# Kernel optimization log

Hardware: AMD Instinct MI355X
Metric: run time of the kernel (lower is better)

The kernel has to match this reference:

```python
import jax, jax.numpy as jnp
import numpy as np

D = 128; H = 4; C = 128; L = 4
NC = 65536   # cells (1024 graphs x 64 cells)
NP = 32768   # pieces
NE = 65536   # edges per cell->cell direction
B = 1024     # num graphs
BW = 7       # BOARD_WIDTH (undefined global in source; connect-four width)
SLOPE = 0.2  # GATv2 LeakyReLU negative slope


def setup_inputs() -> dict:
    key = jax.random.key(0)
    ks = jax.random.split(key, 24)
    s = 0.05
    return {
        'cell_x': jnp.zeros((NC,), dtype=jnp.int32),
        'piece_x': jax.random.randint(ks[0], (NP,), 0, 2, dtype=jnp.int32),
        'occ_src': jax.random.randint(ks[1], (NP,), 0, NP, dtype=jnp.int32),
        'occ_dst': jax.random.randint(ks[2], (NP,), 0, NC, dtype=jnp.int32),
        'en_src': jax.random.randint(ks[3], (NE,), 0, NC, dtype=jnp.int32),
        'en_dst': jax.random.randint(ks[4], (NE,), 0, NC, dtype=jnp.int32),
        'ee_src': jax.random.randint(ks[5], (NE,), 0, NC, dtype=jnp.int32),
        'ee_dst': jax.random.randint(ks[6], (NE,), 0, NC, dtype=jnp.int32),
        'cell_batch': (jnp.arange(NC, dtype=jnp.int32) // (NC // B)).astype(jnp.int32),
        'cell_emb': jax.random.normal(ks[7], (1, D), jnp.float32),
        'piece_emb': jax.random.normal(ks[8], (2, D), jnp.float32),
        'Wl': jax.random.normal(ks[9], (L, 3, D, H * C), jnp.float32) * s,
        'bl': jnp.zeros((L, 3, H * C), jnp.float32),
        'Wr': jax.random.normal(ks[10], (L, 3, D, H * C), jnp.float32) * s,
        'br': jnp.zeros((L, 3, H * C), jnp.float32),
        'att': jax.random.normal(ks[11], (L, 3, H, C), jnp.float32) * 0.1,
        'conv_bias': jnp.zeros((L, 3, C), jnp.float32),
        'fc1_W': jax.random.normal(ks[12], (D, 64), jnp.float32) * s,
        'fc1_b': jnp.zeros((64,), jnp.float32),
        'pol_W': jax.random.normal(ks[13], (64, BW), jnp.float32) * s,
        'pol_b': jnp.zeros((BW,), jnp.float32),
        'val_W': jax.random.normal(ks[14], (64, 1), jnp.float32) * s,
        'val_b': jnp.zeros((1,), jnp.float32),
    }


def _gatv2(x_src, x_dst, src, dst, Wl, bl, Wr, br, att, bias):
    # PyG GATv2Conv, concat=False (mean over heads), add_self_loops=False, eval-mode dropout.
    n_dst = x_dst.shape[0]
    xl = (x_src @ Wl + bl).reshape(-1, H, C)      # [Ns,H,C]
    xr = (x_dst @ Wr + br).reshape(n_dst, H, C)   # [Nd,H,C]
    e = jax.nn.leaky_relu(xl[src] + xr[dst], SLOPE)            # [E,H,C]
    score = jnp.einsum('ehc,hc->eh', e, att)                   # [E,H]
    m = jax.ops.segment_max(score, dst, num_segments=n_dst)    # [Nd,H]
    p = jnp.exp(score - m[dst])
    denom = jax.ops.segment_sum(p, dst, num_segments=n_dst)
    alpha = p / (denom[dst] + 1e-16)                           # scatter-softmax
    out = jax.ops.segment_sum(alpha[:, :, None] * xl[src], dst, num_segments=n_dst)  # [Nd,H,C]
    return out.mean(axis=1) + bias


def reference(cell_x, piece_x, occ_src, occ_dst, en_src, en_dst, ee_src, ee_dst,
              cell_batch, cell_emb, piece_emb, Wl, bl, Wr, br, att, conv_bias,
              fc1_W, fc1_b, pol_W, pol_b, val_W, val_b):
    cell = cell_emb[cell_x]    # [NC,D]
    piece = piece_emb[piece_x]  # [NP,D]
    rels = [(occ_src, occ_dst), (en_src, en_dst), (ee_src, ee_dst)]
    for l in range(L):
        acc = jnp.zeros_like(cell)
        for r, (src, dst) in enumerate(rels):
            x_src = piece if r == 0 else cell
            acc = acc + _gatv2(x_src, cell, src, dst, Wl[l, r], bl[l, r],
                               Wr[l, r], br[l, r], att[l, r], conv_bias[l, r])
        cell = jax.nn.relu(acc)  # HeteroConv aggr='sum', then relu; dropout is identity in eval
    # global mean pool over cells per graph
    sums = jax.ops.segment_sum(cell, cell_batch, num_segments=B)
    cnts = jax.ops.segment_sum(jnp.ones((cell.shape[0],), cell.dtype), cell_batch, num_segments=B)
    pooled = sums / jnp.maximum(cnts, 1.0)[:, None]            # [B,D]
    h = jax.nn.relu(pooled @ fc1_W + fc1_b)
    policy_logits = h @ pol_W + pol_b
    value = jnp.tanh(h @ val_W + val_b)
    return policy_logits, value
```

## Files before the change

kernel.cpp:

```cpp
#include <hip/hip_runtime.h>
#include <hip/hip_bf16.h>
#include <math.h>

#define NCELLS 65536
#define NPIECE 32768
#define NEDGE  65536
#define NGRAPH 1024
#define DIM    128
#define NH     4
#define CH     128
#define HC     512
#define NLAYER 4
#define SLOPE  0.2f
#define DCAP   16

#define SCAP0   16384
#define SCAP12  36864
#define HCAP0   8192
#define HCAP12  20480
#define XLC_OFF0 0
#define XLC_OFF1 16384
#define XLC_OFF2 53248
#define XRC_OFF0 0
#define XRC_OFF1 8192
#define XRC_OFF2 28672
#define YL_OFF0  0
#define YL_OFF1  32768
#define YL_OFF2  98304
#define GEMM_BLOCKS 5632

typedef __attribute__((ext_vector_type(8))) __bf16 bf16x8;
typedef __attribute__((ext_vector_type(4))) float f32x4;

__device__ inline float bf2f(unsigned int u) {
    return __uint_as_float(u << 16);
}
__device__ inline unsigned short f2bf(float f) {
    unsigned int x = __float_as_uint(f);
    unsigned int r = (x + 0x7fff + ((x >> 16) & 1)) >> 16;
    return (unsigned short)r;
}

#define GLOBAL_AS __attribute__((address_space(1)))
#define LDS_AS __attribute__((address_space(3)))
__device__ __forceinline__ void async_cp16(const void* g, void* l) {
    __builtin_amdgcn_global_load_lds((const GLOBAL_AS unsigned int*)g,
                                     (LDS_AS unsigned int*)l, 16, 0, 0);
}

__global__ void fill_kernel(float* __restrict__ p, float v, long n) {
    long i = (long)blockIdx.x * 256 + threadIdx.x;
    if (i < n) p[i] = v;
}

__global__ void embed_bf16_kernel(const int* __restrict__ idx, const float* __restrict__ emb,
                                  unsigned short* __restrict__ outb) {
    long t = (long)blockIdx.x * 256 + threadIdx.x;
    int node = (int)(t >> 7);
    int c = (int)(t & 127);
    outb[t] = f2bf(emb[(size_t)idx[node] * DIM + c]);
}

__global__ __launch_bounds__(256) void wconv_kernel(const float* __restrict__ Wl,
                                                    const float* __restrict__ Wr,
                                                    unsigned short* __restrict__ Wt) {
    __shared__ float tile[16][17];
    int bid = blockIdx.x;
    int wi = bid >> 8;
    int rem = bid & 255;
    int kt = rem >> 5;
    int nt = rem & 31;
    int tx = threadIdx.x & 15, ty = threadIdx.x >> 4;
    const float* W = (wi < 12) ? (Wl + (size_t)wi * DIM * HC) : (Wr + (size_t)(wi - 12) * DIM * HC);
    tile[ty][tx] = W[(size_t)(kt * 16 + ty) * HC + nt * 16 + tx];
    __syncthreads();
    Wt[(size_t)wi * HC * DIM + (size_t)(nt * 16 + ty) * DIM + kt * 16 + tx] = f2bf(tile[tx][ty]);
}

__global__ __launch_bounds__(256) void wsum_kernel(const float* __restrict__ Wl,
                                                   const float* __restrict__ bl,
                                                   unsigned short* __restrict__ Wsumt,
                                                   float* __restrict__ bsum) {
    int wi = blockIdx.x;
    const float* W = Wl + (size_t)wi * DIM * HC;
    for (int base = 0; base < 16384; base += 256) {
        int idx = base + threadIdx.x;
        int c = idx & 127, k = idx >> 7;
        float s = 0.25f * (W[(size_t)k * HC + c] + W[(size_t)k * HC + 128 + c] +
                           W[(size_t)k * HC + 256 + c] + W[(size_t)k * HC + 384 + c]);
        Wsumt[(size_t)wi * 16384 + (size_t)c * 128 + k] = f2bf(s);
    }
    if (threadIdx.x < 128) {
        int c = threadIdx.x;
        const float* b = bl + (size_t)wi * HC;
        bsum[wi * 128 + c] = 0.25f * (b[c] + b[128 + c] + b[256 + c] + b[384 + c]);
    }
}

__global__ __launch_bounds__(256) void bucket_build(const int* __restrict__ occ_src,
                                                    const int* __restrict__ occ_dst,
                                                    const int* __restrict__ en_src,
                                                    const int* __restrict__ en_dst,
                                                    const int* __restrict__ ee_src,
                                                    const int* __restrict__ ee_dst,
                                                    int* __restrict__ cnt3,
                                                    int* __restrict__ bucket3) {
    int id = blockIdx.x * 256 + threadIdx.x;
    int rel, e;
    const int* dstp;
    const int* srcp;
    if (id < NPIECE) { rel = 0; e = id; dstp = occ_dst; srcp = occ_src; }
    else if (id < NPIECE + NEDGE) { rel = 1; e = id - NPIECE; dstp = en_dst; srcp = en_src; }
    else if (id < NPIECE + 2 * NEDGE) { rel = 2; e = id - NPIECE - NEDGE; dstp = ee_dst; srcp = ee_src; }
    else return;
    int d = dstp[e];
    int pos = atomicAdd(&cnt3[rel * NCELLS + d], 1);
    if (pos < DCAP) bucket3[(size_t)rel * NCELLS * DCAP + (size_t)d * DCAP + pos] = srcp[e];
}

__global__ __launch_bounds__(256) void srcmark_build(const int* __restrict__ occ_src,
                                                     const int* __restrict__ occ_dst,
                                                     const int* __restrict__ en_src,
                                                     const int* __restrict__ en_dst,
                                                     const int* __restrict__ ee_src,
                                                     const int* __restrict__ ee_dst,
                                                     const int* __restrict__ cnt3,
                                                     int* __restrict__ srcmark) {
    int id = blockIdx.x * 256 + threadIdx.x;
    int rel, e;
    const int* dstp;
    const int* srcp;
    if (id < NPIECE) { rel = 0; e = id; dstp = occ_dst; srcp = occ_src; }
    else if (id < NPIECE + NEDGE) { rel = 1; e = id - NPIECE; dstp = en_dst; srcp = en_src; }
    else if (id < NPIECE + 2 * NEDGE) { rel = 2; e = id - NPIECE - NEDGE; dstp = ee_dst; srcp = ee_src; }
    else return;
    if (cnt3[rel * NCELLS + dstp[e]] >= 2) srcmark[(rel << 16) + srcp[e]] = 1;
}

__global__ __launch_bounds__(256) void hot_build(const int* __restrict__ cnt3,
                                                 int* __restrict__ counts,
                                                 int* __restrict__ hotlist,
                                                 int* __restrict__ hotpos) {
    int id = blockIdx.x * 256 + threadIdx.x;
    if (id >= 3 * NCELLS) return;
    int lane = threadIdx.x & 63;
    int r = id >> 16;
    int cap  = (r == 0) ? HCAP0 : HCAP12;
    int loff = (r == 0) ? XRC_OFF0 : (r == 1) ? XRC_OFF1 : XRC_OFF2;
    bool active = (cnt3[id] >= 2);
    unsigned long long mask = __ballot(active);
    if (mask) {
        int base = 0;
        if (lane == 0) base = atomicAdd(&counts[r], __popcll(mask));
        base = __shfl(base, 0, 64);
        if (active) {
            int pos = base + (int)__popcll(mask & ((1ull << lane) - 1ull));
            if (pos < cap) {
                hotlist[loff + pos] = id & (NCELLS - 1);
                hotpos[id] = pos;
            } else {
                hotpos[id] = cap - 1;
            }
        }
    }
}

__global__ __launch_bounds__(256) void src_compact(const int* __restrict__ srcmark,
                                                   int* __restrict__ counts,
                                                   int* __restrict__ srclist,
                                                   int* __restrict__ srcpos) {
    int id = blockIdx.x * 256 + threadIdx.x;
    if (id >= 3 * NCELLS) return;
    int lane = threadIdx.x & 63;
    int r = id >> 16;
    int cap  = (r == 0) ? SCAP0 : SCAP12;
    int loff = (r == 0) ? XLC_OFF0 : (r == 1) ? XLC_OFF1 : XLC_OFF2;
    bool active = (srcmark[id] != 0);
    unsigned long long mask = __ballot(active);
    if (mask) {
        int base = 0;
        if (lane == 0) base = atomicAdd(&counts[4 + r], __popcll(mask));
        base = __shfl(base, 0, 64);
        if (active) {
            int pos = base + (int)__popcll(mask & ((1ull << lane) - 1ull));
            if (pos < cap) {
                srclist[loff + pos] = id & (NCELLS - 1);
                srcpos[id] = pos;
            } else {
                srcpos[id] = cap - 1;
            }
        }
    }
}

__device__ __forceinline__ void gemm_body(const unsigned short* __restrict__ A,
                                          const int* __restrict__ gather, int nrows,
                                          const unsigned short* __restrict__ Bt,
                                          const float* __restrict__ bias,
                                          unsigned short* __restrict__ out, int ostride,
                                          int row0, int col0,
                                          unsigned short* smem) {
    unsigned short* As = smem;
    unsigned short* Bs = smem + 16384;
    const int t = threadIdx.x;
    const int w = t >> 6;
    const int l = t & 63;
    const int q = l >> 4, r15 = l & 15;

    {
#pragma unroll
        for (int it = 0; it < 8; it++) {
            int r0 = 32 * w + 4 * it;
            int row = r0 + q;
            int c = r15 ^ (row & 15);
            int grow = row0 + row;
            if (gather) grow = gather[grow < nrows ? grow : (nrows - 1)];
            async_cp16(A + (size_t)grow * 128 + c * 8, &As[r0 * 128]);
        }
        const unsigned short* Bg = Bt + (size_t)col0 * 128;
#pragma unroll
        for (int it = 0; it < 4; it++) {
            int r0 = 16 * w + 4 * it;
            int row = r0 + q;
            int c = r15 ^ (row & 15);
            async_cp16(Bg + (size_t)row * 128 + c * 8, &Bs[r0 * 128]);
        }
    }
    __syncthreads();

    const int m0 = (w >> 1) * 64;
    const int n0 = (w & 1) * 32;

    f32x4 acc[2][4][2];
#pragma unroll
    for (int nh = 0; nh < 2; nh++)
#pragma unroll
        for (int i = 0; i < 4; i++)
#pragma unroll
            for (int j = 0; j < 2; j++) acc[nh][i][j] = (f32x4)(0.0f);

#pragma unroll
    for (int ks = 0; ks < 4; ks++) {
        int slot = (4 * ks + q) ^ r15;
        bf16x8 a[4], b[2];
#pragma unroll
        for (int i = 0; i < 4; i++)
            a[i] = *(const bf16x8*)&As[(m0 + 16 * i + r15) * 128 + slot * 8];
#pragma unroll
        for (int j = 0; j < 2; j++)
            b[j] = *(const bf16x8*)&Bs[(n0 + 16 * j + r15) * 128 + slot * 8];
#pragma unroll
        for (int i = 0; i < 4; i++)
#pragma unroll
            for (int j = 0; j < 2; j++)
                acc[0][i][j] = __builtin_amdgcn_mfma_f32_16x16x32_bf16(a[i], b[j], acc[0][i][j], 0, 0, 0);
    }
    __syncthreads();

    {
        const unsigned short* Bg = Bt + (size_t)(col0 + 64) * 128;
#pragma unroll
        for (int it = 0; it < 4; it++) {
            int r0 = 16 * w + 4 * it;
            int row = r0 + q;
            int c = r15 ^ (row & 15);
            async_cp16(Bg + (size_t)row * 128 + c * 8, &Bs[r0 * 128]);
        }
    }
    __syncthreads();

#pragma unroll
    for (int ks = 0; ks < 4; ks++) {
        int slot = (4 * ks + q) ^ r15;
        bf16x8 a[4], b[2];
#pragma unroll
        for (int i = 0; i < 4; i++)
            a[i] = *(const bf16x8*)&As[(m0 + 16 * i + r15) * 128 + slot * 8];
#pragma unroll
        for (int j = 0; j < 2; j++)
            b[j] = *(const bf16x8*)&Bs[(n0 + 16 * j + r15) * 128 + slot * 8];
#pragma unroll
        for (int i = 0; i < 4; i++)
#pragma unroll
            for (int j = 0; j < 2; j++)
                acc[1][i][j] = __builtin_amdgcn_mfma_f32_16x16x32_bf16(a[i], b[j], acc[1][i][j], 0, 0, 0);
    }
    __syncthreads();

    unsigned short* tile = smem;
#pragma unroll
    for (int nh = 0; nh < 2; nh++)
#pragma unroll
        for (int j = 0; j < 2; j++) {
            int col = nh * 64 + n0 + 16 * j + r15;
            float bv = bias[col0 + col];
#pragma unroll
            for (int i = 0; i < 4; i++) {
                int mg = m0 + 16 * i + 4 * q;
#pragma unroll
                for (int rg = 0; rg < 4; rg++)
                    tile[(mg + rg) * 136 + col] = f2bf(acc[nh][i][j][rg] + bv);
            }
        }
    __syncthreads();
#pragma unroll
    for (int it = 0; it < 8; it++) {
        int rr = it * 16 + (t >> 4);
        int cc = (t & 15) * 8;
        if (row0 + rr < nrows) {
            uint4 v = *(const uint4*)&tile[rr * 136 + cc];
            *(uint4*)&out[(size_t)(row0 + rr) * ostride + col0 + cc] = v;
        }
    }
}

__global__ __launch_bounds__(256) void gemm_layer(const unsigned short* __restrict__ pieceb,
                                                  const unsigned short* __restrict__ cellb,
                                                  const int* __restrict__ srclist,
                                                  const int* __restrict__ hotlist,
                                                  const int* __restrict__ counts,
                                                  const unsigned short* __restrict__ Wt,
                                                  const unsigned short* __restrict__ Wsumt,
                                                  const float* __restrict__ bl,
                                                  const float* __restrict__ br,
                                                  const float* __restrict__ bsum,
                                                  unsigned short* __restrict__ xlc,
                                                  unsigned short* __restrict__ yl,
                                                  unsigned short* __restrict__ xrc,
                                                  int lay) {
    __shared__ unsigned short smem[24576];
    int x = blockIdx.x;
    int r, sec, idx;
    if (x < 1024) {
        r = 0;
        if (x < 512) { sec = 0; idx = x; }
        else if (x < 768) { sec = 1; idx = x - 512; }
        else { sec = 2; idx = x - 768; }
    } else if (x < 3328) {
        r = 1; x -= 1024;
        if (x < 1152) { sec = 0; idx = x; }
        else if (x < 1664) { sec = 1; idx = x - 1152; }
        else { sec = 2; idx = x - 1664; }
    } else {
        r = 2; x -= 3328;
        if (x < 1152) { sec = 0; idx = x; }
        else if (x < 1664) { sec = 1; idx = x - 1152; }
        else { sec = 2; idx = x - 1664; }
    }
    int wi = lay * 3 + r;
    const unsigned short* Asrc = (r == 0) ? pieceb : cellb;
    int Ns = (r == 0) ? NPIECE : NCELLS;
    int scap = (r == 0) ? SCAP0 : SCAP12;
    int hcap = (r == 0) ? HCAP0 : HCAP12;
    int xlcoff = (r == 0) ? XLC_OFF0 : (r == 1) ? XLC_OFF1 : XLC_OFF2;
    int xrcoff = (r == 0) ? XRC_OFF0 : (r == 1) ? XRC_OFF1 : XRC_OFF2;
    int yloff  = (r == 0) ? YL_OFF0  : (r == 1) ? YL_OFF1  : YL_OFF2;

    if (sec == 0) {
        int nrowblk = scap >> 7;
        int row = idx % nrowblk, col = idx / nrowblk;
        int nsrc = counts[4 + r];
        if (nsrc > scap) nsrc = scap;
        if (row * 128 >= nsrc) return;
        gemm_body(Asrc, srclist + xlcoff, nsrc,
                  Wt + (size_t)wi * HC * DIM, bl + (size_t)wi * HC,
                  xlc + (size_t)xlcoff * HC, HC, row * 128, col * 128, smem);
    } else if (sec == 1) {
        gemm_body(Asrc, nullptr, Ns,
                  Wsumt + (size_t)wi * 16384, bsum + (size_t)wi * 128,
                  yl + (size_t)yloff * 128, 128, idx * 128, 0, smem);
    } else {
        int nrowblk = hcap >> 7;
        int row = idx % nrowblk, col = idx / nrowblk;
        int nhot = counts[r];
        if (nhot > hcap) nhot = hcap;
        if (row * 128 >= nhot) return;
        gemm_body(cellb, hotlist + xrcoff, nhot,
                  Wt + (size_t)(12 + wi) * HC * DIM, br + (size_t)wi * HC,
                  xrc + (size_t)xrcoff * HC, HC, row * 128, col * 128, smem);
    }
}

__global__ __launch_bounds__(256) void agg3(const unsigned short* __restrict__ xlc,
                                            const unsigned short* __restrict__ yl,
                                            const unsigned short* __restrict__ xrc,
                                            const int* __restrict__ bucket3,
                                            const int* __restrict__ cnt3,
                                            const int* __restrict__ hotpos,
                                            const int* __restrict__ srcpos,
                                            const float* __restrict__ att,
                                            const float* __restrict__ cb,
                                            unsigned short* __restrict__ cellb,
                                            int lay) {
    int d = blockIdx.x * 4 + (threadIdx.x >> 6);
    int l = threadIdx.x & 63;

    float acc[8] = {0.f, 0.f, 0.f, 0.f, 0.f, 0.f, 0.f, 0.f};
#pragma unroll
    for (int r = 0; r < 3; r++) {
        int deg = cnt3[r * NCELLS + d];
        if (deg > DCAP) deg = DCAP;
        if (deg == 0) continue;
        const int* bucket = bucket3 + (size_t)r * NCELLS * DCAP + (size_t)d * DCAP;
        int xlcoff = (r == 0) ? XLC_OFF0 : (r == 1) ? XLC_OFF1 : XLC_OFF2;
        int xrcoff = (r == 0) ? XRC_OFF0 : (r == 1) ? XRC_OFF1 : XRC_OFF2;
        int yloff  = (r == 0) ? YL_OFF0  : (r == 1) ? YL_OFF1  : YL_OFF2;

        if (deg == 1) {
            if (l < 16) {
                int s = bucket[0];
                uint4 v = *(const uint4*)(yl + (size_t)(yloff + s) * 128 + l * 8);
                acc[0] += bf2f(v.x & 0xffff); acc[1] += bf2f(v.x >> 16);
                acc[2] += bf2f(v.y & 0xffff); acc[3] += bf2f(v.y >> 16);
                acc[4] += bf2f(v.z & 0xffff); acc[5] += bf2f(v.z >> 16);
                acc[6] += bf2f(v.w & 0xffff); acc[7] += bf2f(v.w >> 16);
            }
        } else {
            int hp = hotpos[r * NCELLS + d];
            uint4 rv = *(const uint4*)(xrc + (size_t)(xrcoff + hp) * HC + l * 8);
            float re[8];
            re[0] = bf2f(rv.x & 0xffff); re[1] = bf2f(rv.x >> 16);
            re[2] = bf2f(rv.y & 0xffff); re[3] = bf2f(rv.y >> 16);
            re[4] = bf2f(rv.z & 0xffff); re[5] = bf2f(rv.z >> 16);
            re[6] = bf2f(rv.w & 0xffff); re[7] = bf2f(rv.w >> 16);
            const float* at = att + (size_t)(lay * 3 + r) * HC;
            float4 a0 = *(const float4*)&at[l * 8];
            float4 a1 = *(const float4*)&at[l * 8 + 4];
            float av[8] = {a0.x, a0.y, a0.z, a0.w, a1.x, a1.y, a1.z, a1.w};

            int spv = (l < deg) ? srcpos[r * NCELLS + bucket[l]] : 0;

            float sc_slot = -3.0e38f;
            for (int k = 0; k < deg; k++) {
                int sp = __shfl(spv, k, 64);
                uint4 v = *(const uint4*)(xlc + (size_t)(xlcoff + sp) * HC + l * 8);
                float le[8];
                le[0] = bf2f(v.x & 0xffff); le[1] = bf2f(v.x >> 16);
                le[2] = bf2f(v.y & 0xffff); le[3] = bf2f(v.y >> 16);
                le[4] = bf2f(v.z & 0xffff); le[5] = bf2f(v.z >> 16);
                le[6] = bf2f(v.w & 0xffff); le[7] = bf2f(v.w >> 16);
                float partial = 0.f;
#pragma unroll
                for (int j = 0; j < 8; j++) {
                    float e = le[j] + re[j];
                    e = e > 0.0f ? e : SLOPE * e;
                    partial += e * av[j];
                }
#pragma unroll
                for (int off = 1; off < 16; off <<= 1) partial += __shfl_xor(partial, off, 64);
                if ((l & 15) == k) sc_slot = partial;
            }

            float mx = sc_slot;
#pragma unroll
            for (int off = 1; off < 16; off <<= 1) mx = fmaxf(mx, __shfl_xor(mx, off, 64));
            float p = ((l & 15) < deg) ? expf(sc_slot - mx) : 0.f;
            float sm = p;
#pragma unroll
            for (int off = 1; off < 16; off <<= 1) sm += __shfl_xor(sm, off, 64);
            float al_slot = p / (sm + 1e-16f) * 0.25f;

            float tm[8] = {0.f, 0.f, 0.f, 0.f, 0.f, 0.f, 0.f, 0.f};
            for (int k = 0; k < deg; k++) {
                int sp = __shfl(spv, k, 64);
                float a = __shfl(al_slot, (l & 48) | k, 64);
                uint4 v = *(const uint4*)(xlc + (size_t)(xlcoff + sp) * HC + l * 8);
                tm[0] += a * bf2f(v.x & 0xffff); tm[1] += a * bf2f(v.x >> 16);
                tm[2] += a * bf2f(v.y & 0xffff); tm[3] += a * bf2f(v.y >> 16);
                tm[4] += a * bf2f(v.z & 0xffff); tm[5] += a * bf2f(v.z >> 16);
                tm[6] += a * bf2f(v.w & 0xffff); tm[7] += a * bf2f(v.w >> 16);
            }
#pragma unroll
            for (int j = 0; j < 8; j++) {
                tm[j] += __shfl_xor(tm[j], 16, 64);
                tm[j] += __shfl_xor(tm[j], 32, 64);
                acc[j] += tm[j];
            }
        }
    }

    if (l < 16) {
        int c0 = l * 8;
        float v[8];
#pragma unroll
        for (int j = 0; j < 8; j++) {
            int c = c0 + j;
            float b = cb[c] + cb[CH + c] + cb[2 * CH + c];
            v[j] = fmaxf(acc[j] + b, 0.0f);
        }
        uint4 pv;
        pv.x = (unsigned)f2bf(v[0]) | ((unsigned)f2bf(v[1]) << 16);
        pv.y = (unsigned)f2bf(v[2]) | ((unsigned)f2bf(v[3]) << 16);
        pv.z = (unsigned)f2bf(v[4]) | ((unsigned)f2bf(v[5]) << 16);
        pv.w = (unsigned)f2bf(v[6]) | ((unsigned)f2bf(v[7]) << 16);
        *(uint4*)&cellb[(size_t)d * CH + c0] = pv;
    }
}

__global__ __launch_bounds__(64) void pool_kernel(const unsigned short* __restrict__ cellb,
                                                  float* __restrict__ pooled) {
    int b = blockIdx.x, l = threadIdx.x;
    const unsigned short* base = cellb + (size_t)b * 64 * DIM;
    float s[8] = {0.f, 0.f, 0.f, 0.f, 0.f, 0.f, 0.f, 0.f};
    for (int i = 0; i < 64; i++) {
        uint4 v = *(const uint4*)(base + (size_t)i * DIM + (l & 15) * 8);
        s[0] += bf2f(v.x & 0xffff); s[1] += bf2f(v.x >> 16);
        s[2] += bf2f(v.y & 0xffff); s[3] += bf2f(v.y >> 16);
        s[4] += bf2f(v.z & 0xffff); s[5] += bf2f(v.z >> 16);
        s[6] += bf2f(v.w & 0xffff); s[7] += bf2f(v.w >> 16);
    }
    if (l < 16) {
        float4 o0 = make_float4(s[0] * (1.f / 64.f), s[1] * (1.f / 64.f),
                                s[2] * (1.f / 64.f), s[3] * (1.f / 64.f));
        float4 o1 = make_float4(s[4] * (1.f / 64.f), s[5] * (1.f / 64.f),
                                s[6] * (1.f / 64.f), s[7] * (1.f / 64.f));
        *(float4*)&pooled[(size_t)b * DIM + l * 8] = o0;
        *(float4*)&pooled[(size_t)b * DIM + l * 8 + 4] = o1;
    }
}

__global__ __launch_bounds__(64) void head_kernel(const float* __restrict__ pooled,
                                                  const float* __restrict__ fc1W,
                                                  const float* __restrict__ fc1b,
                                                  const float* __restrict__ polW,
                                                  const float* __restrict__ polb,
                                                  const float* __restrict__ valW,
                                                  const float* __restrict__ valb,
                                                  float* __restrict__ out) {
    int b = blockIdx.x, t = threadIdx.x;
    __shared__ float ps[128];
    __shared__ float hs[64];
    ps[t] = pooled[(size_t)b * DIM + t];
    ps[t + 64] = pooled[(size_t)b * DIM + 64 + t];
    __syncthreads();
    float h = fc1b[t];
#pragma unroll 16
    for (int d = 0; d < 128; d++) h += ps[d] * fc1W[d * 64 + t];
    hs[t] = fmaxf(h, 0.0f);
    __syncthreads();
    if (t < 7) {
        float po = polb[t];
#pragma unroll 16
        for (int k = 0; k < 64; k++) po += hs[k] * polW[k * 7 + t];
        out[(size_t)b * 7 + t] = po;
    }
    if (t == 63) {
        float v = valb[0];
#pragma unroll 16
        for (int k = 0; k < 64; k++) v += hs[k] * valW[k];
        out[(size_t)NGRAPH * 7 + b] = tanhf(v);
    }
}

extern "C" void kernel_launch(void* const* d_in, const int* in_sizes, int n_in,
                              void* d_out, int out_size, void* d_ws, size_t ws_size,
                              hipStream_t stream) {
    const int* cell_x   = (const int*)d_in[0];
    const int* piece_x  = (const int*)d_in[1];
    const int* occ_src  = (const int*)d_in[2];
    const int* occ_dst  = (const int*)d_in[3];
    const int* en_src   = (const int*)d_in[4];
    const int* en_dst   = (const int*)d_in[5];
    const int* ee_src   = (const int*)d_in[6];
    const int* ee_dst   = (const int*)d_in[7];
    const float* cell_emb  = (const float*)d_in[9];
    const float* piece_emb = (const float*)d_in[10];
    const float* Wl  = (const float*)d_in[11];
    const float* bl  = (const float*)d_in[12];
    const float* Wr  = (const float*)d_in[13];
    const float* br  = (const float*)d_in[14];
    const float* att = (const float*)d_in[15];
    const float* conv_bias = (const float*)d_in[16];
    const float* fc1W = (const float*)d_in[17];
    const float* fc1b = (const float*)d_in[18];
    const float* polW = (const float*)d_in[19];
    const float* polb = (const float*)d_in[20];
    const float* valW = (const float*)d_in[21];
    const float* valb = (const float*)d_in[22];
    float* out = (float*)d_out;

    char* ws = (char*)d_ws;
    size_t off = 0;
    auto take = [&](size_t bytes) -> void* {
        void* p = (void*)(ws + off);
        off += (bytes + 255) & ~(size_t)255;
        return p;
    };
    unsigned short* cellb  = (unsigned short*)take((size_t)NCELLS * DIM * 2);
    unsigned short* pieceb = (unsigned short*)take((size_t)NPIECE * DIM * 2);
    unsigned short* xlc    = (unsigned short*)take((size_t)(SCAP0 + 2 * SCAP12) * HC * 2);
    unsigned short* yl     = (unsigned short*)take((size_t)(NPIECE + 2 * NCELLS) * 128 * 2);
    unsigned short* xrc    = (unsigned short*)take((size_t)(HCAP0 + 2 * HCAP12) * HC * 2);
    unsigned short* Wt     = (unsigned short*)take((size_t)24 * HC * DIM * 2);
    unsigned short* Wsumt  = (unsigned short*)take((size_t)12 * 128 * 128 * 2);
    float* bsum            = (float*)take((size_t)12 * 128 * 4);
    int*   izone   = (int*)take(((size_t)6 * NCELLS + 8) * 4);
    int*   cnt3    = izone;
    int*   counts  = izone + 3 * NCELLS;
    int*   srcmark = izone + 3 * NCELLS + 8;
    int*   bucket3 = (int*)take((size_t)3 * NCELLS * DCAP * 4);
    int*   hotlist = (int*)take((size_t)(HCAP0 + 2 * HCAP12) * 4);
    int*   hotpos  = (int*)take((size_t)3 * NCELLS * 4);
    int*   srclist = (int*)take((size_t)(SCAP0 + 2 * SCAP12) * 4);
    int*   srcpos  = (int*)take((size_t)3 * NCELLS * 4);
    float* pooled  = (float*)take((size_t)NGRAPH * DIM * 4);

    if (off > ws_size) {
        fill_kernel<<<(out_size + 255) / 256, 256, 0, stream>>>(out, 0.0f, out_size);
        return;
    }

    wconv_kernel<<<24 * 256, 256, 0, stream>>>(Wl, Wr, Wt);
    wsum_kernel<<<12, 256, 0, stream>>>(Wl, bl, Wsumt, bsum);
    embed_bf16_kernel<<<NPIECE * DIM / 256, 256, 0, stream>>>(piece_x, piece_emb, pieceb);
    embed_bf16_kernel<<<NCELLS * DIM / 256, 256, 0, stream>>>(cell_x, cell_emb, cellb);
    fill_kernel<<<(6 * NCELLS + 8 + 255) / 256, 256, 0, stream>>>((float*)izone, 0.0f, 6 * NCELLS + 8);
    bucket_build<<<(NPIECE + 2 * NEDGE + 255) / 256, 256, 0, stream>>>(
        occ_src, occ_dst, en_src, en_dst, ee_src, ee_dst, cnt3, bucket3);
    hot_build<<<(3 * NCELLS + 255) / 256, 256, 0, stream>>>(cnt3, counts, hotlist, hotpos);
    srcmark_build<<<(NPIECE + 2 * NEDGE + 255) / 256, 256, 0, stream>>>(
        occ_src, occ_dst, en_src, en_dst, ee_src, ee_dst, cnt3, srcmark);
    src_compact<<<(3 * NCELLS + 255) / 256, 256, 0, stream>>>(srcmark, counts, srclist, srcpos);

    for (int l = 0; l < NLAYER; l++) {
        gemm_layer<<<GEMM_BLOCKS, 256, 0, stream>>>(
            pieceb, cellb, srclist, hotlist, counts, Wt, Wsumt, bl, br, bsum,
            xlc, yl, xrc, l);
        agg3<<<NCELLS / 4, 256, 0, stream>>>(
            xlc, yl, xrc, bucket3, cnt3, hotpos, srcpos, att,
            conv_bias + (size_t)l * 3 * CH, cellb, l);
    }

    pool_kernel<<<NGRAPH, 64, 0, stream>>>(cellb, pooled);
    head_kernel<<<NGRAPH, 64, 0, stream>>>(pooled, fc1W, fc1b, polW, polb, valW, valb, out);
}
```

Before: 764.4 us.

## Compact degree-one source rows for summed-weight GEMM and prefetch neighbor rows

Sources that feed only degree-1 destinations are now marked and compacted into a ylist, so the summed-weight GEMM section runs only over those rows instead of every source node. The aggregation kernel indexes the compacted yl buffer through ypos. It also preloads the first four neighbor xlc rows into registers and reuses them for the score and weighted-sum passes, instead of loading them twice. This adds a marking output, a compaction kernel and a larger zero-fill. Capacity limits (YCAP) clamp overflow to the last slot, which is only correct if the graph stays within those caps.

```diff
diff --git a/kernel.cpp b/kernel.cpp
--- a/kernel.cpp
+++ b/kernel.cpp
@@ -18,6 +18,8 @@
 #define SCAP12  36864
 #define HCAP0   8192
 #define HCAP12  20480
+#define YCAP0   20480
+#define YCAP12  28672
 #define XLC_OFF0 0
 #define XLC_OFF1 16384
 #define XLC_OFF2 53248
@@ -25,9 +27,9 @@
 #define XRC_OFF1 8192
 #define XRC_OFF2 28672
 #define YL_OFF0  0
-#define YL_OFF1  32768
-#define YL_OFF2  98304
-#define GEMM_BLOCKS 5632
+#define YL_OFF1  20480
+#define YL_OFF2  49152
+#define GEMM_BLOCKS 4960
 
 typedef __attribute__((ext_vector_type(8))) __bf16 bf16x8;
 typedef __attribute__((ext_vector_type(4))) float f32x4;
@@ -39,6 +41,12 @@
     unsigned int x = __float_as_uint(f);
     unsigned int r = (x + 0x7fff + ((x >> 16) & 1)) >> 16;
     return (unsigned short)r;
+}
+__device__ __forceinline__ void unpack8(uint4 v, float* o) {
+    o[0] = bf2f(v.x & 0xffff); o[1] = bf2f(v.x >> 16);
+    o[2] = bf2f(v.y & 0xffff); o[3] = bf2f(v.y >> 16);
+    o[4] = bf2f(v.z & 0xffff); o[5] = bf2f(v.z >> 16);
+    o[6] = bf2f(v.w & 0xffff); o[7] = bf2f(v.w >> 16);
 }
 
 #define GLOBAL_AS __attribute__((address_space(1)))
@@ -118,14 +126,15 @@
     if (pos < DCAP) bucket3[(size_t)rel * NCELLS * DCAP + (size_t)d * DCAP + pos] = srcp[e];
 }
 
-__global__ __launch_bounds__(256) void srcmark_build(const int* __restrict__ occ_src,
-                                                     const int* __restrict__ occ_dst,
-                                                     const int* __restrict__ en_src,
-                                                     const int* __restrict__ en_dst,
-                                                     const int* __restrict__ ee_src,
-                                                     const int* __restrict__ ee_dst,
-                                                     const int* __restrict__ cnt3,
-                                                     int* __restrict__ srcmark) {
+__global__ __launch_bounds__(256) void mark_build(const int* __restrict__ occ_src,
+                                                  const int* __restrict__ occ_dst,
+                                                  const int* __restrict__ en_src,
+                                                  const int* __restrict__ en_dst,
+                                                  const int* __restrict__ ee_src,
+                                                  const int* __restrict__ ee_dst,
+                                                  const int* __restrict__ cnt3,
+                                                  int* __restrict__ srcmark,
+                                                  int* __restrict__ ymark) {
     int id = blockIdx.x * 256 + threadIdx.x;
     int rel, e;
     const int* dstp;
@@ -134,7 +143,9 @@
     else if (id < NPIECE + NEDGE) { rel = 1; e = id - NPIECE; dstp = en_dst; srcp = en_src; }
     else if (id < NPIECE + 2 * NEDGE) { rel = 2; e = id - NPIECE - NEDGE; dstp = ee_dst; srcp = ee_src; }
     else return;
-    if (cnt3[rel * NCELLS + dstp[e]] >= 2) srcmark[(rel << 16) + srcp[e]] = 1;
+    int c = cnt3[rel * NCELLS + dstp[e]];
+    if (c >= 2) srcmark[(rel << 16) + srcp[e]] = 1;
+    else ymark[(rel << 16) + srcp[e]] = 1;
 }
 
 __global__ __launch_bounds__(256) void hot_build(const int* __restrict__ cnt3,
@@ -193,6 +204,34 @@
     }
 }
 
+__global__ __launch_bounds__(256) void y_compact(const int* __restrict__ ymark,
+                                                 int* __restrict__ counts,
+                                                 int* __restrict__ ylist,
+                                                 int* __restrict__ ypos) {
+    int id = blockIdx.x * 256 + threadIdx.x;
+    if (id >= 3 * NCELLS) return;
+    int lane = threadIdx.x & 63;
+    int r = id >> 16;
+    int cap  = (r == 0) ? YCAP0 : YCAP12;
+    int loff = (r == 0) ? YL_OFF0 : (r == 1) ? YL_OFF1 : YL_OFF2;
+    bool active = (ymark[id] != 0);
+    unsigned long long mask = __ballot(active);
+    if (mask) {
+        int base = 0;
+        if (lane == 0) base = atomicAdd(&counts[8 + r], __popcll(mask));
+        base = __shfl(base, 0, 64);
+        if (active) {
+            int pos = base + (int)__popcll(mask & ((1ull << lane) - 1ull));
+            if (pos < cap) {
+                ylist[loff + pos] = id & (NCELLS - 1);
+                ypos[id] = pos;
+            } else {
+                ypos[id] = cap - 1;
+            }
+        }
+    }
+}
+
 __device__ __forceinline__ void gemm_body(const unsigned short* __restrict__ A,
                                           const int* __restrict__ gather, int nrows,
                                           const unsigned short* __restrict__ Bt,
@@ -318,6 +357,7 @@
                                                   const unsigned short* __restrict__ cellb,
                                                   const int* __restrict__ srclist,
                                                   const int* __restrict__ hotlist,
+                                                  const int* __restrict__ ylist,
                                                   const int* __restrict__ counts,
                                                   const unsigned short* __restrict__ Wt,
                                                   const unsigned short* __restrict__ Wsumt,
@@ -331,27 +371,27 @@
     __shared__ unsigned short smem[24576];
     int x = blockIdx.x;
     int r, sec, idx;
-    if (x < 1024) {
+    if (x < 928) {
         r = 0;
         if (x < 512) { sec = 0; idx = x; }
-        else if (x < 768) { sec = 1; idx = x - 512; }
-        else { sec = 2; idx = x - 768; }
-    } else if (x < 3328) {
-        r = 1; x -= 1024;
+        else if (x < 672) { sec = 1; idx = x - 512; }
+        else { sec = 2; idx = x - 672; }
+    } else if (x < 2944) {
+        r = 1; x -= 928;
         if (x < 1152) { sec = 0; idx = x; }
-        else if (x < 1664) { sec = 1; idx = x - 1152; }
-        else { sec = 2; idx = x - 1664; }
+        else if (x < 1376) { sec = 1; idx = x - 1152; }
+        else { sec = 2; idx = x - 1376; }
     } else {
-        r = 2; x -= 3328;
+        r = 2; x -= 2944;
         if (x < 1152) { sec = 0; idx = x; }
-        else if (x < 1664) { sec = 1; idx = x - 1152; }
-        else { sec = 2; idx = x - 1664; }
+        else if (x < 1376) { sec = 1; idx = x - 1152; }
+        else { sec = 2; idx = x - 1376; }
     }
     int wi = lay * 3 + r;
     const unsigned short* Asrc = (r == 0) ? pieceb : cellb;
-    int Ns = (r == 0) ? NPIECE : NCELLS;
     int scap = (r == 0) ? SCAP0 : SCAP12;
     int hcap = (r == 0) ? HCAP0 : HCAP12;
+    int ycap = (r == 0) ? YCAP0 : YCAP12;
     int xlcoff = (r == 0) ? XLC_OFF0 : (r == 1) ? XLC_OFF1 : XLC_OFF2;
     int xrcoff = (r == 0) ? XRC_OFF0 : (r == 1) ? XRC_OFF1 : XRC_OFF2;
     int yloff  = (r == 0) ? YL_OFF0  : (r == 1) ? YL_OFF1  : YL_OFF2;
@@ -366,7 +406,10 @@
                   Wt + (size_t)wi * HC * DIM, bl + (size_t)wi * HC,
                   xlc + (size_t)xlcoff * HC, HC, row * 128, col * 128, smem);
     } else if (sec == 1) {
-        gemm_body(Asrc, nullptr, Ns,
+        int ny = counts[8 + r];
+        if (ny > ycap) ny = ycap;
+        if (idx * 128 >= ny) return;
+        gemm_body(Asrc, ylist + yloff, ny,
                   Wsumt + (size_t)wi * 16384, bsum + (size_t)wi * 128,
                   yl + (size_t)yloff * 128, 128, idx * 128, 0, smem);
     } else {
@@ -388,6 +431,7 @@
                                             const int* __restrict__ cnt3,
                                             const int* __restrict__ hotpos,
                                             const int* __restrict__ srcpos,
+                                            const int* __restrict__ ypos,
                                             const float* __restrict__ att,
                                             const float* __restrict__ cb,
                                             unsigned short* __restrict__ cellb,
@@ -408,21 +452,18 @@
 
         if (deg == 1) {
             if (l < 16) {
-                int s = bucket[0];
-                uint4 v = *(const uint4*)(yl + (size_t)(yloff + s) * 128 + l * 8);
-                acc[0] += bf2f(v.x & 0xffff); acc[1] += bf2f(v.x >> 16);
-                acc[2] += bf2f(v.y & 0xffff); acc[3] += bf2f(v.y >> 16);
-                acc[4] += bf2f(v.z & 0xffff); acc[5] += bf2f(v.z >> 16);
-                acc[6] += bf2f(v.w & 0xffff); acc[7] += bf2f(v.w >> 16);
+                int yp = ypos[r * NCELLS + bucket[0]];
+                uint4 v = *(const uint4*)(yl + (size_t)(yloff + yp) * 128 + l * 8);
+                float y[8];
+                unpack8(v, y);
+#pragma unroll
+                for (int j = 0; j < 8; j++) acc[j] += y[j];
             }
         } else {
             int hp = hotpos[r * NCELLS + d];
             uint4 rv = *(const uint4*)(xrc + (size_t)(xrcoff + hp) * HC + l * 8);
             float re[8];
-            re[0] = bf2f(rv.x & 0xffff); re[1] = bf2f(rv.x >> 16);
-            re[2] = bf2f(rv.y & 0xffff); re[3] = bf2f(rv.y >> 16);
-            re[4] = bf2f(rv.z & 0xffff); re[5] = bf2f(rv.z >> 16);
-            re[6] = bf2f(rv.w & 0xffff); re[7] = bf2f(rv.w >> 16);
+            unpack8(rv, re);
             const float* at = att + (size_t)(lay * 3 + r) * HC;
             float4 a0 = *(const float4*)&at[l * 8];
             float4 a1 = *(const float4*)&at[l * 8 + 4];
@@ -430,15 +471,38 @@
 
             int spv = (l < deg) ? srcpos[r * NCELLS + bucket[l]] : 0;
 
+            uint4 cv[4];
+#pragma unroll
+            for (int k = 0; k < 4; k++) {
+                if (k < deg) {
+                    int sp = __shfl(spv, k, 64);
+                    cv[k] = *(const uint4*)(xlc + (size_t)(xlcoff + sp) * HC + l * 8);
+                }
+            }
+
             float sc_slot = -3.0e38f;
-            for (int k = 0; k < deg; k++) {
+#pragma unroll
+            for (int k = 0; k < 4; k++) {
+                if (k < deg) {
+                    float le[8];
+                    unpack8(cv[k], le);
+                    float partial = 0.f;
+#pragma unroll
+                    for (int j = 0; j < 8; j++) {
+                        float e = le[j] + re[j];
+                        e = e > 0.0f ? e : SLOPE * e;
+                        partial += e * av[j];
+                    }
+#pragma unroll
+                    for (int off = 1; off < 16; off <<= 1) partial += __shfl_xor(partial, off, 64);
+                    if ((l & 15) == k) sc_slot = partial;
+                }
+            }
+            for (int k = 4; k < deg; k++) {
                 int sp = __shfl(spv, k, 64);
                 uint4 v = *(const uint4*)(xlc + (size_t)(xlcoff + sp) * HC + l * 8);
                 float le[8];
-                le[0] = bf2f(v.x & 0xffff); le[1] = bf2f(v.x >> 16);
-                le[2] = bf2f(v.y & 0xffff); le[3] = bf2f(v.y >> 16);
-                le[4] = bf2f(v.z & 0xffff); le[5] = bf2f(v.z >> 16);
-                le[6] = bf2f(v.w & 0xffff); le[7] = bf2f(v.w >> 16);
+                unpack8(v, le);
                 float partial = 0.f;
 #pragma unroll
                 for (int j = 0; j < 8; j++) {
@@ -461,14 +525,24 @@
             float al_slot = p / (sm + 1e-16f) * 0.25f;
 
             float tm[8] = {0.f, 0.f, 0.f, 0.f, 0.f, 0.f, 0.f, 0.f};
-            for (int k = 0; k < deg; k++) {
+#pragma unroll
+            for (int k = 0; k < 4; k++) {
+                if (k < deg) {
+                    float a = __shfl(al_slot, (l & 48) | k, 64);
+                    float le[8];
+                    unpack8(cv[k], le);
+#pragma unroll
+                    for (int j = 0; j < 8; j++) tm[j] += a * le[j];
+                }
+            }
+            for (int k = 4; k < deg; k++) {
                 int sp = __shfl(spv, k, 64);
                 float a = __shfl(al_slot, (l & 48) | k, 64);
                 uint4 v = *(const uint4*)(xlc + (size_t)(xlcoff + sp) * HC + l * 8);
-                tm[0] += a * bf2f(v.x & 0xffff); tm[1] += a * bf2f(v.x >> 16);
-                tm[2] += a * bf2f(v.y & 0xffff); tm[3] += a * bf2f(v.y >> 16);
-                tm[4] += a * bf2f(v.z & 0xffff); tm[5] += a * bf2f(v.z >> 16);
-                tm[6] += a * bf2f(v.w & 0xffff); tm[7] += a * bf2f(v.w >> 16);
+                float le[8];
+                unpack8(v, le);
+#pragma unroll
+                for (int j = 0; j < 8; j++) tm[j] += a * le[j];
             }
 #pragma unroll
             for (int j = 0; j < 8; j++) {
@@ -504,10 +578,10 @@
     float s[8] = {0.f, 0.f, 0.f, 0.f, 0.f, 0.f, 0.f, 0.f};
     for (int i = 0; i < 64; i++) {
         uint4 v = *(const uint4*)(base + (size_t)i * DIM + (l & 15) * 8);
-        s[0] += bf2f(v.x & 0xffff); s[1] += bf2f(v.x >> 16);
-        s[2] += bf2f(v.y & 0xffff); s[3] += bf2f(v.y >> 16);
-        s[4] += bf2f(v.z & 0xffff); s[5] += bf2f(v.z >> 16);
-        s[6] += bf2f(v.w & 0xffff); s[7] += bf2f(v.w >> 16);
+        float y[8];
+        unpack8(v, y);
+#pragma unroll
+        for (int j = 0; j < 8; j++) s[j] += y[j];
     }
     if (l < 16) {
         float4 o0 = make_float4(s[0] * (1.f / 64.f), s[1] * (1.f / 64.f),
@@ -589,20 +663,23 @@
     unsigned short* cellb  = (unsigned short*)take((size_t)NCELLS * DIM * 2);
     unsigned short* pieceb = (unsigned short*)take((size_t)NPIECE * DIM * 2);
     unsigned short* xlc    = (unsigned short*)take((size_t)(SCAP0 + 2 * SCAP12) * HC * 2);
-    unsigned short* yl     = (unsigned short*)take((size_t)(NPIECE + 2 * NCELLS) * 128 * 2);
+    unsigned short* yl     = (unsigned short*)take((size_t)(YCAP0 + 2 * YCAP12) * 128 * 2);
     unsigned short* xrc    = (unsigned short*)take((size_t)(HCAP0 + 2 * HCAP12) * HC * 2);
     unsigned short* Wt     = (unsigned short*)take((size_t)24 * HC * DIM * 2);
     unsigned short* Wsumt  = (unsigned short*)take((size_t)12 * 128 * 128 * 2);
     float* bsum            = (float*)take((size_t)12 * 128 * 4);
-    int*   izone   = (int*)take(((size_t)6 * NCELLS + 8) * 4);
+    int*   izone   = (int*)take(((size_t)9 * NCELLS + 16) * 4);
     int*   cnt3    = izone;
     int*   counts  = izone + 3 * NCELLS;
-    int*   srcmark = izone + 3 * NCELLS + 8;
+    int*   srcmark = izone + 3 * NCELLS + 16;
+    int*   ymark   = izone + 6 * NCELLS + 16;
     int*   bucket3 = (int*)take((size_t)3 * NCELLS * DCAP * 4);
     int*   hotlist = (int*)take((size_t)(HCAP0 + 2 * HCAP12) * 4);
     int*   hotpos  = (int*)take((size_t)3 * NCELLS * 4);
     int*   srclist = (int*)take((size_t)(SCAP0 + 2 * SCAP12) * 4);
     int*   srcpos  = (int*)take((size_t)3 * NCELLS * 4);
+    int*   ylist   = (int*)take((size_t)(YCAP0 + 2 * YCAP12) * 4);
+    int*   ypos    = (int*)take((size_t)3 * NCELLS * 4);
     float* pooled  = (float*)take((size_t)NGRAPH * DIM * 4);
 
     if (off > ws_size) {
@@ -614,20 +691,21 @@
     wsum_kernel<<<12, 256, 0, stream>>>(Wl, bl, Wsumt, bsum);
     embed_bf16_kernel<<<NPIECE * DIM / 256, 256, 0, stream>>>(piece_x, piece_emb, pieceb);
     embed_bf16_kernel<<<NCELLS * DIM / 256, 256, 0, stream>>>(cell_x, cell_emb, cellb);
-    fill_kernel<<<(6 * NCELLS + 8 + 255) / 256, 256, 0, stream>>>((float*)izone, 0.0f, 6 * NCELLS + 8);
+    fill_kernel<<<(9 * NCELLS + 16 + 255) / 256, 256, 0, stream>>>((float*)izone, 0.0f, 9 * NCELLS + 16);
     bucket_build<<<(NPIECE + 2 * NEDGE + 255) / 256, 256, 0, stream>>>(
         occ_src, occ_dst, en_src, en_dst, ee_src, ee_dst, cnt3, bucket3);
     hot_build<<<(3 * NCELLS + 255) / 256, 256, 0, stream>>>(cnt3, counts, hotlist, hotpos);
-    srcmark_build<<<(NPIECE + 2 * NEDGE + 255) / 256, 256, 0, stream>>>(
-        occ_src, occ_dst, en_src, en_dst, ee_src, ee_dst, cnt3, srcmark);
+    mark_build<<<(NPIECE + 2 * NEDGE + 255) / 256, 256, 0, stream>>>(
+        occ_src, occ_dst, en_src, en_dst, ee_src, ee_dst, cnt3, srcmark, ymark);
     src_compact<<<(3 * NCELLS + 255) / 256, 256, 0, stream>>>(srcmark, counts, srclist, srcpos);
+    y_compact<<<(3 * NCELLS + 255) / 256, 256, 0, stream>>>(ymark, counts, ylist, ypos);
 
     for (int l = 0; l < NLAYER; l++) {
         gemm_layer<<<GEMM_BLOCKS, 256, 0, stream>>>(
-            pieceb, cellb, srclist, hotlist, counts, Wt, Wsumt, bl, br, bsum,
+            pieceb, cellb, srclist, hotlist, ylist, counts, Wt, Wsumt, bl, br, bsum,
             xlc, yl, xrc, l);
         agg3<<<NCELLS / 4, 256, 0, stream>>>(
-            xlc, yl, xrc, bucket3, cnt3, hotpos, srcpos, att,
+            xlc, yl, xrc, bucket3, cnt3, hotpos, srcpos, ypos, att,
             conv_bias + (size_t)l * 3 * CH, cellb, l);
     }
 
```

After: 882.9 us. +15.5%, slower.
